# Performance work log

Hardware: AMD Instinct MI355X
Metric: run time of the kernel (lower is better)

The kernel has to match this reference:

```python
import jax, jax.numpy as jnp
import numpy as np

TOP_K = 8  # num_experts_per_tok


def setup_inputs() -> dict:
    key = jax.random.key(0)
    k1, k2 = jax.random.split(key)
    hidden_states = jax.random.normal(k1, (4, 4096, 2048), dtype=jnp.float32)
    weight = jax.random.normal(k2, (128, 2048), dtype=jnp.float32) * 0.02
    return {"hidden_states": hidden_states, "weight": weight}


def reference(hidden_states, weight):
    B, S, H = hidden_states.shape
    x = hidden_states.reshape(-1, H).astype(jnp.float32)        # [T, H], T = B*S
    logits = jnp.einsum("th,eh->te", x, weight.astype(jnp.float32))  # [T, E]
    scores = jax.nn.softmax(logits, axis=-1)                    # float32 softmax
    topk_weight, topk_idx = jax.lax.top_k(scores, TOP_K)        # [T, K]
    # norm_topk_prob=True: renormalize selected probabilities
    topk_weight = topk_weight / jnp.sum(topk_weight, axis=-1, keepdims=True)
    return topk_idx, topk_weight
```

## Files before the change

kernel.cpp:

```cpp
#include <hip/hip_runtime.h>
#include <math.h>

#define T_TOKENS 16384
#define HDIM     2048
#define NEXP     128
#define TOPK     8

#define KSPLIT   4
#define KRANGE   (HDIM / KSPLIT)
#define BKC      32
#define NCHUNK   (KRANGE / BKC)

#define F16_MIN_NORM    6.1035156e-05f
#define SPLIT_SCALE     4096.0f
#define INV_SPLIT_SCALE 2.44140625e-04f

typedef __attribute__((ext_vector_type(8))) _Float16 f16x8;
typedef __attribute__((ext_vector_type(4))) float    f32x4;

__device__ __forceinline__ void f16split(float f, _Float16& hi, _Float16& lo) {
    _Float16 h = (_Float16)f;
    float back = (float)h;
    if (fabsf(f) < F16_MIN_NORM) { h = (_Float16)0.f; back = 0.f; }
    lo = (_Float16)((f - back) * SPLIT_SCALE);
    hi = h;
}

__global__ __launch_bounds__(256) void split_w(const float* __restrict__ w,
                                               unsigned short* __restrict__ w1,
                                               unsigned short* __restrict__ w2) {
    int i = blockIdx.x * 256 + threadIdx.x;
    _Float16 h, l;
    f16split(w[i], h, l);
    union { _Float16 x; unsigned short u; } ch, cl;
    ch.x = h; cl.x = l;
    w1[i] = ch.u; w2[i] = cl.u;
}

__global__ __launch_bounds__(256, 2) void moe_gate(const float* __restrict__ x,
                                                   const unsigned short* __restrict__ w1,
                                                   const unsigned short* __restrict__ w2,
                                                   float* __restrict__ out_idx,
                                                   float* __restrict__ out_w) {
    __shared__ float epil[KSPLIT][32][132];

    const int tid  = threadIdx.x;
    const int lane = tid & 63;
    const int wv   = tid >> 6;
    const int col  = lane & 15;
    const int quad = lane >> 4;
    const long tok0 = (long)blockIdx.x * 32;
    const int kbase = wv * KRANGE;

    f32x4 acc[2][8], accc[2][8];
#pragma unroll
    for (int m = 0; m < 2; ++m)
#pragma unroll
        for (int n = 0; n < 8; ++n) { acc[m][n] = (f32x4){0,0,0,0}; accc[m][n] = (f32x4){0,0,0,0}; }

    const float* xr0 = x + (tok0 + col) * HDIM + kbase + quad * 8;
    const float* xr1 = xr0 + 16 * HDIM;
    const unsigned short* wp1 = w1 + (size_t)col * HDIM + kbase + quad * 8;
    const unsigned short* wp2 = w2 + (size_t)col * HDIM + kbase + quad * 8;

    float4 xa[4];
    xa[0] = *(const float4*)(xr0);     xa[1] = *(const float4*)(xr0 + 4);
    xa[2] = *(const float4*)(xr1);     xa[3] = *(const float4*)(xr1 + 4);

    for (int ch = 0; ch < NCHUNK; ++ch) {
        f16x8 a1[2], a2[2];
#pragma unroll
        for (int m = 0; m < 2; ++m) {
            const float* f = (const float*)&xa[2 * m];
#pragma unroll
            for (int j = 0; j < 8; ++j) {
                _Float16 h, l;
                f16split(f[j], h, l);
                a1[m][j] = h; a2[m][j] = l;
            }
        }
        if (ch + 1 < NCHUNK) {
            const float* p0 = xr0 + (ch + 1) * BKC;
            const float* p1 = xr1 + (ch + 1) * BKC;
            xa[0] = *(const float4*)(p0); xa[1] = *(const float4*)(p0 + 4);
            xa[2] = *(const float4*)(p1); xa[3] = *(const float4*)(p1 + 4);
        }

        const unsigned short* b1p = wp1 + ch * BKC;
        const unsigned short* b2p = wp2 + ch * BKC;
#pragma unroll
        for (int nt = 0; nt < 8; ++nt) {
            f16x8 b1 = *(const f16x8*)(b1p + (size_t)nt * 16 * HDIM);
            f16x8 b2 = *(const f16x8*)(b2p + (size_t)nt * 16 * HDIM);
            acc[0][nt]  = __builtin_amdgcn_mfma_f32_16x16x32_f16(a1[0], b1, acc[0][nt],  0, 0, 0);
            acc[1][nt]  = __builtin_amdgcn_mfma_f32_16x16x32_f16(a1[1], b1, acc[1][nt],  0, 0, 0);
            accc[0][nt] = __builtin_amdgcn_mfma_f32_16x16x32_f16(a1[0], b2, accc[0][nt], 0, 0, 0);
            accc[0][nt] = __builtin_amdgcn_mfma_f32_16x16x32_f16(a2[0], b1, accc[0][nt], 0, 0, 0);
            accc[1][nt] = __builtin_amdgcn_mfma_f32_16x16x32_f16(a1[1], b2, accc[1][nt], 0, 0, 0);
            accc[1][nt] = __builtin_amdgcn_mfma_f32_16x16x32_f16(a2[1], b1, accc[1][nt], 0, 0, 0);
        }
    }

#pragma unroll
    for (int m = 0; m < 2; ++m)
#pragma unroll
        for (int nt = 0; nt < 8; ++nt)
#pragma unroll
            for (int r = 0; r < 4; ++r)
                epil[wv][m * 16 + quad * 4 + r][nt * 16 + col] =
                    acc[m][nt][r] + accc[m][nt][r] * INV_SPLIT_SCALE;
    __syncthreads();

    for (int i = 0; i < 8; ++i) {
        const int t = wv * 8 + i;
        float v0 = 0.f, v1 = 0.f;
#pragma unroll
        for (int q = 0; q < KSPLIT; ++q) {
            float2 p = *(const float2*)(&epil[q][t][2 * lane]);
            v0 += p.x; v1 += p.y;
        }
        const int i0 = 2 * lane, i1 = 2 * lane + 1;

        float topv[TOPK];
        int topi[TOPK];
#pragma unroll
        for (int s = 0; s < TOPK; ++s) {
            float mv = (v0 >= v1) ? v0 : v1;
            int   mi = (v0 >= v1) ? i0 : i1;
#pragma unroll
            for (int off = 32; off >= 1; off >>= 1) {
                float ov = __shfl_xor(mv, off);
                int   oi = __shfl_xor(mi, off);
                if (ov > mv || (ov == mv && oi < mi)) { mv = ov; mi = oi; }
            }
            topv[s] = mv; topi[s] = mi;
            if (i0 == mi) v0 = -INFINITY;
            if (i1 == mi) v1 = -INFINITY;
        }

        const float m = topv[0];
        float sum = 0.f;
#pragma unroll
        for (int s = 0; s < TOPK; ++s) sum += expf(topv[s] - m);
        const float inv = 1.f / sum;

        float myv = topv[0]; int myi = topi[0];
#pragma unroll
        for (int s = 1; s < TOPK; ++s)
            if (lane == s) { myv = topv[s]; myi = topi[s]; }

        if (lane < TOPK) {
            long tok = tok0 + t;
            out_idx[tok * TOPK + lane] = (float)myi;
            out_w[tok * TOPK + lane]   = expf(myv - m) * inv;
        }
    }
}

extern "C" void kernel_launch(void* const* d_in, const int* in_sizes, int n_in,
                              void* d_out, int out_size, void* d_ws, size_t ws_size,
                              hipStream_t stream) {
    const float* x = (const float*)d_in[0];
    const float* w = (const float*)d_in[1];
    float* out = (float*)d_out;

    unsigned short* w1 = (unsigned short*)d_ws;
    unsigned short* w2 = w1 + (size_t)NEXP * HDIM;

    split_w<<<(NEXP * HDIM) / 256, 256, 0, stream>>>(w, w1, w2);
    moe_gate<<<T_TOKENS / 32, 256, 0, stream>>>(x, w1, w2, out, out + (size_t)T_TOKENS * TOPK);
}
```

Before: 280.4 us.

## Split experts across waves with LDS-staged x tile and MFMA-packed weights

Waves now split the 128 experts instead of splitting the K dimension. Each block loads and converts its 32-token x tile once into double-buffered LDS as f16 hi/lo parts and shares it across the four waves. Weights are pre-packed into MFMA fragment order so each lane does one contiguous 16-byte load, and the cross-wave K reduction in the epilogue goes away. In exchange the kernel adds a barrier per 64-wide K chunk and LDS read traffic. Each wave now issues fewer MFMAs per chunk, which may leave less work to hide latency.

```diff
diff --git a/kernel.cpp b/kernel.cpp
--- a/kernel.cpp
+++ b/kernel.cpp
@@ -6,10 +6,9 @@
 #define NEXP     128
 #define TOPK     8
 
-#define KSPLIT   4
-#define KRANGE   (HDIM / KSPLIT)
-#define BKC      32
-#define NCHUNK   (KRANGE / BKC)
+#define BK    64
+#define NCH   (HDIM / BK)
+#define KPAD  72
 
 #define F16_MIN_NORM    6.1035156e-05f
 #define SPLIT_SCALE     4096.0f
@@ -26,23 +25,38 @@
     hi = h;
 }
 
-__global__ __launch_bounds__(256) void split_w(const float* __restrict__ w,
-                                               unsigned short* __restrict__ w1,
-                                               unsigned short* __restrict__ w2) {
-    int i = blockIdx.x * 256 + threadIdx.x;
-    _Float16 h, l;
-    f16split(w[i], h, l);
-    union { _Float16 x; unsigned short u; } ch, cl;
-    ch.x = h; cl.x = l;
-    w1[i] = ch.u; w2[i] = cl.u;
+__global__ __launch_bounds__(256) void pack_w(const float* __restrict__ w,
+                                              unsigned short* __restrict__ wp1,
+                                              unsigned short* __restrict__ wp2) {
+    int p = blockIdx.x * 256 + threadIdx.x;
+    int lane = p & 63, nt = (p >> 6) & 7, kk = p >> 9;
+    int col = lane & 15, quad = lane >> 4;
+    const float* src = w + (size_t)(nt * 16 + col) * HDIM + kk * 32 + quad * 8;
+    unsigned short h[8], l[8];
+#pragma unroll
+    for (int j = 0; j < 8; ++j) {
+        _Float16 hh, ll;
+        f16split(src[j], hh, ll);
+        union { _Float16 x; unsigned short u; } ch, cl;
+        ch.x = hh; cl.x = ll;
+        h[j] = ch.u; l[j] = cl.u;
+    }
+    *(uint4*)(wp1 + (size_t)p * 8) = *(const uint4*)h;
+    *(uint4*)(wp2 + (size_t)p * 8) = *(const uint4*)l;
 }
 
 __global__ __launch_bounds__(256, 2) void moe_gate(const float* __restrict__ x,
-                                                   const unsigned short* __restrict__ w1,
-                                                   const unsigned short* __restrict__ w2,
+                                                   const unsigned short* __restrict__ wp1,
+                                                   const unsigned short* __restrict__ wp2,
                                                    float* __restrict__ out_idx,
                                                    float* __restrict__ out_w) {
-    __shared__ float epil[KSPLIT][32][132];
+    __shared__ __align__(16) unsigned char smem[18432];
+    unsigned short* xbuf[2][2];
+    xbuf[0][0] = (unsigned short*)smem;
+    xbuf[0][1] = (unsigned short*)(smem + 4608);
+    xbuf[1][0] = (unsigned short*)(smem + 9216);
+    xbuf[1][1] = (unsigned short*)(smem + 13824);
+    float* epil = (float*)smem;
 
     const int tid  = threadIdx.x;
     const int lane = tid & 63;
@@ -50,75 +64,93 @@
     const int col  = lane & 15;
     const int quad = lane >> 4;
     const long tok0 = (long)blockIdx.x * 32;
-    const int kbase = wv * KRANGE;
-
-    f32x4 acc[2][8], accc[2][8];
+
+    const int srow = tid >> 3, scol = (tid & 7) * 8;
+    const float* xg = x + (tok0 + srow) * HDIM + scol;
+    const int swoff = srow * KPAD + scol;
+
+    f32x4 acc[2][2], accc[2][2];
 #pragma unroll
     for (int m = 0; m < 2; ++m)
 #pragma unroll
-        for (int n = 0; n < 8; ++n) { acc[m][n] = (f32x4){0,0,0,0}; accc[m][n] = (f32x4){0,0,0,0}; }
-
-    const float* xr0 = x + (tok0 + col) * HDIM + kbase + quad * 8;
-    const float* xr1 = xr0 + 16 * HDIM;
-    const unsigned short* wp1 = w1 + (size_t)col * HDIM + kbase + quad * 8;
-    const unsigned short* wp2 = w2 + (size_t)col * HDIM + kbase + quad * 8;
-
-    float4 xa[4];
-    xa[0] = *(const float4*)(xr0);     xa[1] = *(const float4*)(xr0 + 4);
-    xa[2] = *(const float4*)(xr1);     xa[3] = *(const float4*)(xr1 + 4);
-
-    for (int ch = 0; ch < NCHUNK; ++ch) {
-        f16x8 a1[2], a2[2];
-#pragma unroll
-        for (int m = 0; m < 2; ++m) {
-            const float* f = (const float*)&xa[2 * m];
-#pragma unroll
-            for (int j = 0; j < 8; ++j) {
-                _Float16 h, l;
-                f16split(f[j], h, l);
-                a1[m][j] = h; a2[m][j] = l;
+        for (int n = 0; n < 2; ++n) { acc[m][n] = (f32x4){0,0,0,0}; accc[m][n] = (f32x4){0,0,0,0}; }
+
+    float4 xv0, xv1;
+
+    auto cvt_store = [&](int buf) {
+        const float f[8] = {xv0.x, xv0.y, xv0.z, xv0.w, xv1.x, xv1.y, xv1.z, xv1.w};
+        unsigned short h[8], l[8];
+#pragma unroll
+        for (int j = 0; j < 8; ++j) {
+            _Float16 hh, ll;
+            f16split(f[j], hh, ll);
+            union { _Float16 x; unsigned short u; } ch, cl;
+            ch.x = hh; cl.x = ll;
+            h[j] = ch.u; l[j] = cl.u;
+        }
+        *(uint4*)(xbuf[buf][0] + swoff) = *(const uint4*)h;
+        *(uint4*)(xbuf[buf][1] + swoff) = *(const uint4*)l;
+    };
+
+    xv0 = *(const float4*)(xg);
+    xv1 = *(const float4*)(xg + 4);
+    cvt_store(0);
+    __syncthreads();
+
+    for (int ch = 0; ch < NCH; ++ch) {
+        const int cur = ch & 1;
+        if (ch + 1 < NCH) {
+            xv0 = *(const float4*)(xg + (ch + 1) * BK);
+            xv1 = *(const float4*)(xg + (ch + 1) * BK + 4);
+        }
+
+        f16x8 b1[2][2], b2[2][2];
+#pragma unroll
+        for (int ks = 0; ks < 2; ++ks)
+#pragma unroll
+            for (int n = 0; n < 2; ++n) {
+                const size_t off = ((size_t)((2 * ch + ks) * 8 + (wv * 2 + n)) * 64 + lane) * 8;
+                b1[ks][n] = *(const f16x8*)(wp1 + off);
+                b2[ks][n] = *(const f16x8*)(wp2 + off);
             }
-        }
-        if (ch + 1 < NCHUNK) {
-            const float* p0 = xr0 + (ch + 1) * BKC;
-            const float* p1 = xr1 + (ch + 1) * BKC;
-            xa[0] = *(const float4*)(p0); xa[1] = *(const float4*)(p0 + 4);
-            xa[2] = *(const float4*)(p1); xa[3] = *(const float4*)(p1 + 4);
-        }
-
-        const unsigned short* b1p = wp1 + ch * BKC;
-        const unsigned short* b2p = wp2 + ch * BKC;
-#pragma unroll
-        for (int nt = 0; nt < 8; ++nt) {
-            f16x8 b1 = *(const f16x8*)(b1p + (size_t)nt * 16 * HDIM);
-            f16x8 b2 = *(const f16x8*)(b2p + (size_t)nt * 16 * HDIM);
-            acc[0][nt]  = __builtin_amdgcn_mfma_f32_16x16x32_f16(a1[0], b1, acc[0][nt],  0, 0, 0);
-            acc[1][nt]  = __builtin_amdgcn_mfma_f32_16x16x32_f16(a1[1], b1, acc[1][nt],  0, 0, 0);
-            accc[0][nt] = __builtin_amdgcn_mfma_f32_16x16x32_f16(a1[0], b2, accc[0][nt], 0, 0, 0);
-            accc[0][nt] = __builtin_amdgcn_mfma_f32_16x16x32_f16(a2[0], b1, accc[0][nt], 0, 0, 0);
-            accc[1][nt] = __builtin_amdgcn_mfma_f32_16x16x32_f16(a1[1], b2, accc[1][nt], 0, 0, 0);
-            accc[1][nt] = __builtin_amdgcn_mfma_f32_16x16x32_f16(a2[1], b1, accc[1][nt], 0, 0, 0);
-        }
+
+#pragma unroll
+        for (int ks = 0; ks < 2; ++ks) {
+            f16x8 a1[2], a2[2];
+#pragma unroll
+            for (int m = 0; m < 2; ++m) {
+                const int ao = (m * 16 + col) * KPAD + ks * 32 + quad * 8;
+                a1[m] = *(const f16x8*)(xbuf[cur][0] + ao);
+                a2[m] = *(const f16x8*)(xbuf[cur][1] + ao);
+            }
+#pragma unroll
+            for (int m = 0; m < 2; ++m)
+#pragma unroll
+                for (int n = 0; n < 2; ++n) {
+                    acc[m][n]  = __builtin_amdgcn_mfma_f32_16x16x32_f16(a1[m], b1[ks][n], acc[m][n],  0, 0, 0);
+                    accc[m][n] = __builtin_amdgcn_mfma_f32_16x16x32_f16(a1[m], b2[ks][n], accc[m][n], 0, 0, 0);
+                    accc[m][n] = __builtin_amdgcn_mfma_f32_16x16x32_f16(a2[m], b1[ks][n], accc[m][n], 0, 0, 0);
+                }
+        }
+
+        if (ch + 1 < NCH) cvt_store(cur ^ 1);
+        __syncthreads();
     }
 
 #pragma unroll
     for (int m = 0; m < 2; ++m)
 #pragma unroll
-        for (int nt = 0; nt < 8; ++nt)
+        for (int n = 0; n < 2; ++n)
 #pragma unroll
             for (int r = 0; r < 4; ++r)
-                epil[wv][m * 16 + quad * 4 + r][nt * 16 + col] =
-                    acc[m][nt][r] + accc[m][nt][r] * INV_SPLIT_SCALE;
+                epil[(m * 16 + quad * 4 + r) * 132 + wv * 32 + n * 16 + col] =
+                    acc[m][n][r] + accc[m][n][r] * INV_SPLIT_SCALE;
     __syncthreads();
 
     for (int i = 0; i < 8; ++i) {
         const int t = wv * 8 + i;
-        float v0 = 0.f, v1 = 0.f;
-#pragma unroll
-        for (int q = 0; q < KSPLIT; ++q) {
-            float2 p = *(const float2*)(&epil[q][t][2 * lane]);
-            v0 += p.x; v1 += p.y;
-        }
+        float2 p = *(const float2*)(epil + t * 132 + 2 * lane);
+        float v0 = p.x, v1 = p.y;
         const int i0 = 2 * lane, i1 = 2 * lane + 1;
 
         float topv[TOPK];
@@ -164,9 +196,9 @@
     const float* w = (const float*)d_in[1];
     float* out = (float*)d_out;
 
-    unsigned short* w1 = (unsigned short*)d_ws;
-    unsigned short* w2 = w1 + (size_t)NEXP * HDIM;
-
-    split_w<<<(NEXP * HDIM) / 256, 256, 0, stream>>>(w, w1, w2);
-    moe_gate<<<T_TOKENS / 32, 256, 0, stream>>>(x, w1, w2, out, out + (size_t)T_TOKENS * TOPK);
-}
+    unsigned short* wp1 = (unsigned short*)d_ws;
+    unsigned short* wp2 = wp1 + (size_t)NEXP * HDIM;
+
+    pack_w<<<(64 * 8 * 64) / 256, 256, 0, stream>>>(w, wp1, wp2);
+    moe_gate<<<T_TOKENS / 32, 256, 0, stream>>>(x, wp1, wp2, out, out + (size_t)T_TOKENS * TOPK);
+}
```

New measurement: 264.8 us. 5.6% less time.
